# Kernel tuning notes

Hardware: AMD Instinct MI355X
Metric: run time of the kernel (lower is better)

Reference implementation:

```python
import jax, jax.numpy as jnp
import numpy as np

B, T, D, H = 2, 2048, 1024, 16
DH = D // H
SCALE = DH ** -0.5
NEG_INF = float(np.finfo(np.float32).min)


def setup_inputs() -> dict:
    key = jax.random.key(0)
    ks = jax.random.split(key, 8)
    query = jax.random.normal(ks[0], (B, T, D), dtype=jnp.float32)
    key_t = jax.random.normal(ks[1], (B, T, D), dtype=jnp.float32)
    value = jax.random.normal(ks[2], (B, T, D), dtype=jnp.float32)
    # causal mask: True means blocked (upper triangle)
    mask = ~jnp.tril(jnp.ones((T, T), dtype=bool))
    # key padding: pad tail beyond a random valid length per batch row
    lens = jax.random.randint(ks[3], (B,), T // 2, T)
    key_padding_mask = jnp.arange(T)[None, :] >= lens[:, None]  # [B, T] True = pad
    s = D ** -0.5
    Wq = jax.random.normal(ks[4], (D, D), dtype=jnp.float32) * s
    Wk = jax.random.normal(ks[5], (D, D), dtype=jnp.float32) * s
    Wv = jax.random.normal(ks[6], (D, D), dtype=jnp.float32) * s
    Wo = jax.random.normal(ks[7], (D, D), dtype=jnp.float32) * s
    return {"query": query, "key": key_t, "value": value, "mask": mask,
            "key_padding_mask": key_padding_mask, "Wq": Wq, "Wk": Wk, "Wv": Wv, "Wo": Wo}


def reference(query, key, value, mask, key_padding_mask, Wq, Wk, Wv, Wo):
    # Linear (no bias): y = x @ W.T, then split heads -> [B, H, T, DH]
    def proj(x, W, Tlen):
        return jnp.einsum('btd,ed->bte', x, W).reshape(B, Tlen, H, DH).transpose(0, 2, 1, 3)

    q = proj(query, Wq, T)
    k = proj(key, Wk, T)
    v = proj(value, Wv, T)

    attn = jnp.einsum('bhqd,bhkd->bhqk', q, k) * SCALE  # [B, H, Tq, Tk]
    attn = jnp.where(mask[None, None, :, :], -jnp.inf, attn)
    attn = jnp.where(key_padding_mask[:, None, None, :], -jnp.inf, attn)
    # rows of batches where ALL keys are padding: zero the logits (softmax -> uniform)
    all_masked = jnp.all(key_padding_mask, axis=-1)[:, None, None, None]
    attn = jnp.where(all_masked, 0.0, attn)

    p = jax.nn.softmax(attn, axis=-1)
    p = jnp.where(jnp.isnan(p), 0.0, p)  # scrub NaN rows (all -inf)

    out = jnp.einsum('bhqk,bhkd->bhqd', p, v)
    out = out.transpose(0, 2, 1, 3).reshape(B, T, D)
    return jnp.einsum('btd,ed->bte', out, Wo)
```

## Files before the change

kernel.cpp:

```cpp
#include <hip/hip_runtime.h>

#define B_  2
#define T_  2048
#define D_  1024
#define H_  16
#define DH_ 64
#define M_  4096

typedef _Float16 f16;
typedef _Float16 f16x8 __attribute__((ext_vector_type(8)));
typedef _Float16 f16x4 __attribute__((ext_vector_type(4)));
typedef __fp16   fp16x2 __attribute__((ext_vector_type(2)));
typedef float    f32x4  __attribute__((ext_vector_type(4)));
typedef float    f32x16 __attribute__((ext_vector_type(16)));
typedef unsigned int u32;

__device__ __forceinline__ void async_ld16(const void* g, void* l) {
  __builtin_amdgcn_global_load_lds(
      (const __attribute__((address_space(1))) unsigned int*)g,
      (__attribute__((address_space(3))) unsigned int*)l,
      16, 0, 0);
}

__device__ __forceinline__ u32 pkrtz(float a, float b) {
  union { fp16x2 h; u32 u; } x;
  x.h = __builtin_amdgcn_cvt_pkrtz(a, b);
  return x.u;
}

__global__ __launch_bounds__(256) void convert_all(
    const float* __restrict__ q, const float* __restrict__ k, const float* __restrict__ v,
    const float* __restrict__ wq, const float* __restrict__ wk, const float* __restrict__ wv,
    const float* __restrict__ wo, const void* __restrict__ kpm_raw,
    f16* __restrict__ xh, f16* __restrict__ wh, int* __restrict__ lens_out) {
  int bid = blockIdx.x;
  if (bid >= 8192) {
    int b = bid - 8192;
    __shared__ int s_c8, s_c32;
    if (threadIdx.x == 0) { s_c8 = 0; s_c32 = 0; }
    __syncthreads();
    int tid = threadIdx.x, lane = tid & 63;
    {
      const unsigned char* k8 = (const unsigned char*)kpm_raw + (long)b * T_;
      int cnt = 0;
      for (int j = tid; j < T_; j += 256) cnt += (k8[j] == 0) ? 1 : 0;
#pragma unroll
      for (int off = 1; off < 64; off <<= 1) cnt += __shfl_xor(cnt, off);
      if (lane == 0) atomicAdd(&s_c8, cnt);
    }
    {
      const int* k32 = (const int*)kpm_raw + (long)b * T_;
      int cnt = 0;
      for (int j = tid; j < T_; j += 256) cnt += (k32[j] == 0) ? 1 : 0;
#pragma unroll
      for (int off = 1; off < 64; off <<= 1) cnt += __shfl_xor(cnt, off);
      if (lane == 0) atomicAdd(&s_c32, cnt);
    }
    __syncthreads();
    if (tid == 0) lens_out[b] = (s_c8 == T_) ? s_c32 : s_c8;
    return;
  }
  const float* src;
  f16* dst;
  long base;
  if (bid < 6144) {
    int r = bid >> 11;
    src = (r == 0) ? q : (r == 1) ? k : v;
    dst = xh + (long)r * 4194304;
    base = (long)(bid & 2047) * 2048;
  } else {
    int r = (bid - 6144) >> 9;
    src = (r == 0) ? wq : (r == 1) ? wk : (r == 2) ? wv : wo;
    dst = wh + (long)r * 1048576;
    base = (long)((bid - 6144) & 511) * 2048;
  }
  long e = base + (long)threadIdx.x * 8;
  const float4* s4 = (const float4*)(src + e);
  float4 f0 = s4[0], f1 = s4[1];
  f16x8 o;
  o[0] = (f16)f0.x; o[1] = (f16)f0.y; o[2] = (f16)f0.z; o[3] = (f16)f0.w;
  o[4] = (f16)f1.x; o[5] = (f16)f1.y; o[6] = (f16)f1.z; o[7] = (f16)f1.w;
  *(f16x8*)(dst + e) = o;
}

__global__ __launch_bounds__(256) void gemm_k(
    const f16* __restrict__ Abase, const f16* __restrict__ Wbase,
    f16* __restrict__ Qb, f16* __restrict__ Kb, f16* __restrict__ Vt,
    float* __restrict__ Co, int which) {
  __shared__ __align__(16) f16 As[2][128][32];
  __shared__ __align__(16) f16 Bs[2][128][32];
  const int K = 1024, N = 1024;

  int gx = gridDim.x, gy = gridDim.y;
  int nwg = gx * gy * gridDim.z;
  int bid = blockIdx.x + gx * (blockIdx.y + gy * blockIdx.z);
  int cpx = nwg >> 3;
  int wg = (bid & 7) * cpx + (bid >> 3);
  int bz = wg / (gx * gy);
  int rem = wg - bz * gx * gy;
  int by = rem / gx, bx = rem - by * gx;

  int mode;
  const f16 *A, *W;
  if (which) { mode = 3; A = Abase; W = Wbase; }
  else {
    mode = bz;
    A = Abase + (long)bz * 4194304;
    W = Wbase + (long)bz * 1048576;
  }
  int m0 = by * 128, n0 = bx * 128;
  int tid = threadIdx.x, lane = tid & 63, w = tid >> 6;
  int wm = w >> 1, wn = w & 1;

  int srow = w * 16 + (lane >> 2);
  int scol = (lane & 3) * 8;
  const f16* pa = A + (long)(m0 + srow) * K + scol;
  const f16* pb = W + (long)(n0 + srow) * K + scol;

  f32x4 acc[4][4] = {};
  int row = lane & 15, kq = (lane >> 4) * 8;

  auto STAGE = [&](int k0, int bsel) {
    async_ld16(pa + k0,          &As[bsel][srow][scol]);
    async_ld16(pa + 64 * K + k0, &As[bsel][64 + srow][scol]);
    async_ld16(pb + k0,          &Bs[bsel][srow][scol]);
    async_ld16(pb + 64 * K + k0, &Bs[bsel][64 + srow][scol]);
  };

  STAGE(0, 0);
  asm volatile("s_waitcnt vmcnt(0)" ::: "memory");
  __builtin_amdgcn_s_barrier();

  int cur = 0;
  for (int k0 = 0; k0 < K; k0 += 32) {
    if (k0 + 32 < K) STAGE(k0 + 32, cur ^ 1);
    f16x8 af[4], bfr[4];
#pragma unroll
    for (int m = 0; m < 4; m++) af[m] = *(const f16x8*)&As[cur][wm * 64 + m * 16 + row][kq];
#pragma unroll
    for (int n = 0; n < 4; n++) bfr[n] = *(const f16x8*)&Bs[cur][wn * 64 + n * 16 + row][kq];
#pragma unroll
    for (int m = 0; m < 4; m++)
#pragma unroll
      for (int n = 0; n < 4; n++)
        acc[m][n] = __builtin_amdgcn_mfma_f32_16x16x32_f16(af[m], bfr[n], acc[m][n], 0, 0, 0);
    asm volatile("s_waitcnt vmcnt(0)" ::: "memory");
    __builtin_amdgcn_s_barrier();
    cur ^= 1;
  }

  int r0 = (lane >> 4) * 4;
#pragma unroll
  for (int m = 0; m < 4; m++) {
    int gmb = m0 + wm * 64 + m * 16 + r0;
#pragma unroll
    for (int n = 0; n < 4; n++) {
      int gn = n0 + wn * 64 + n * 16 + row;
      if (mode == 0) {
#pragma unroll
        for (int i = 0; i < 4; i++)
          Qb[(long)(gmb + i) * N + gn] = (f16)(acc[m][n][i] * 0.18033688f);
      } else if (mode == 1) {
#pragma unroll
        for (int i = 0; i < 4; i++)
          Kb[(long)(gmb + i) * N + gn] = (f16)acc[m][n][i];
      } else if (mode == 2) {
        int b = gmb >> 11;
        int t = gmb & 2047;
        int h = gn >> 6, dh = gn & 63;
        f16x4 pk;
#pragma unroll
        for (int i = 0; i < 4; i++) pk[i] = (f16)acc[m][n][i];
        *(f16x4*)&Vt[(long)((b * 16 + h) * 64 + dh) * 2048 + t] = pk;
      } else {
#pragma unroll
        for (int i = 0; i < 4; i++)
          Co[(long)(gmb + i) * N + gn] = acc[m][n][i];
      }
    }
  }
}

__global__ __launch_bounds__(256, 2) void attn_k(
    const f16* __restrict__ Q, const f16* __restrict__ Kp,
    const f16* __restrict__ Vt, const int* __restrict__ Lens,
    f16* __restrict__ Ao) {
  __shared__ __align__(16) f16 Kl[4][4096];
  __shared__ __align__(16) f16 Vl[4][4096];

  int tid = threadIdx.x, lane = tid & 63, w = tid >> 6;
  int bh = blockIdx.x;
  int j  = blockIdx.y;
  int qm = (j < 8) ? (15 - j) : (j - 8);
  int b = bh >> 4, h = bh & 15;
  int r31 = lane & 31, hi = lane >> 5, hi8 = hi * 8;

  int len = Lens[b];
  int q0 = qm * 128;
  int q0w = q0 + w * 32;
  int gq = q0w + r31;

  int blk_kmax = min(q0 + 128, len);
  int wav_kmax = min(q0w + 32, len);
  int NR = (blk_kmax + 127) >> 7;

  const f16* Qh = Q  + (long)b * T_ * D_ + h * 64;
  const f16* Kh = Kp + (long)b * T_ * D_ + h * 64;
  const f16* Vh = Vt + (long)(b * 16 + h) * 64 * T_;

  int srow = w * 16 + (lane >> 3);
  int sc8  = ((lane & 7) ^ ((lane >> 3) & 7)) * 8;
  int ldst = w * 1024 + lane * 8;

  int coff[4];
#pragma unroll
  for (int t = 0; t < 4; t++) coff[t] = ((2 * t + hi) ^ (r31 & 7)) * 8;

  auto STAGE64 = [&](int t, int bsel) {
    int kb = t * 64;
#pragma unroll
    for (int s = 0; s < 2; s++) {
      int row = srow + s * 8;
      async_ld16(Kh + (long)(kb + row) * D_ + sc8, &Kl[bsel][ldst + s * 512]);
      async_ld16(Vh + (long)row * T_ + kb + sc8,   &Vl[bsel][ldst + s * 512]);
    }
  };

  STAGE64(0, 0);
  STAGE64(1, 1);
  f16x8 qf[4];
#pragma unroll
  for (int t = 0; t < 4; t++)
    qf[t] = *(const f16x8*)(Qh + (long)gq * D_ + t * 16 + hi8);

  f32x16 o0 = {}, o1 = {};
  float mrun = -1e30f, lrun = 0.f;

  auto QK = [&](int buf, f32x16& sa, f32x16& sb) {
#pragma unroll
    for (int tq = 0; tq < 4; tq++) {
      f16x8 k0 = *(const f16x8*)&Kl[buf][(r31)      * 64 + coff[tq]];
      f16x8 k1 = *(const f16x8*)&Kl[buf][(32 + r31) * 64 + coff[tq]];
      sa = __builtin_amdgcn_mfma_f32_32x32x16_f16(k0, qf[tq], sa, 0, 0, 0);
      sb = __builtin_amdgcn_mfma_f32_32x32x16_f16(k1, qf[tq], sb, 0, 0, 0);
    }
  };

  auto MASK = [&](f32x16& sa, f32x16& sb, int kb) {
#pragma unroll
    for (int r = 0; r < 16; r++) {
      int pat = (r & 3) + 8 * (r >> 2) + 4 * hi;
      int gk0 = kb + pat, gk1 = kb + 32 + pat;
      if (gk0 > gq || gk0 >= len) sa[r] = -1e30f;
      if (gk1 > gq || gk1 >= len) sb[r] = -1e30f;
    }
  };

  auto PV = [&](int bufV, f32x16& sa, f32x16& sb) {
    u32 a0 = pkrtz(sa[0],  sa[1]),  a1 = pkrtz(sa[2],  sa[3]);
    u32 b0 = pkrtz(sa[4],  sa[5]),  b1 = pkrtz(sa[6],  sa[7]);
    u32 c0 = pkrtz(sa[8],  sa[9]),  c1 = pkrtz(sa[10], sa[11]);
    u32 d0 = pkrtz(sa[12], sa[13]), d1 = pkrtz(sa[14], sa[15]);
    u32 e0 = pkrtz(sb[0],  sb[1]),  e1 = pkrtz(sb[2],  sb[3]);
    u32 f0_ = pkrtz(sb[4],  sb[5]), f1_ = pkrtz(sb[6],  sb[7]);
    u32 g0 = pkrtz(sb[8],  sb[9]),  g1 = pkrtz(sb[10], sb[11]);
    u32 h0 = pkrtz(sb[12], sb[13]), h1 = pkrtz(sb[14], sb[15]);
    asm("v_permlane32_swap_b32 %0, %1" : "+v"(a0), "+v"(b0));
    asm("v_permlane32_swap_b32 %0, %1" : "+v"(a1), "+v"(b1));
    asm("v_permlane32_swap_b32 %0, %1" : "+v"(c0), "+v"(d0));
    asm("v_permlane32_swap_b32 %0, %1" : "+v"(c1), "+v"(d1));
    asm("v_permlane32_swap_b32 %0, %1" : "+v"(e0), "+v"(f0_));
    asm("v_permlane32_swap_b32 %0, %1" : "+v"(e1), "+v"(f1_));
    asm("v_permlane32_swap_b32 %0, %1" : "+v"(g0), "+v"(h0));
    asm("v_permlane32_swap_b32 %0, %1" : "+v"(g1), "+v"(h1));
    union { u32 w[4]; f16x8 v; } f00, f01, f10, f11;
    f00.w[0] = a0;  f00.w[1] = a1;  f00.w[2] = b0;  f00.w[3] = b1;
    f01.w[0] = c0;  f01.w[1] = c1;  f01.w[2] = d0;  f01.w[3] = d1;
    f10.w[0] = e0;  f10.w[1] = e1;  f10.w[2] = f0_; f10.w[3] = f1_;
    f11.w[0] = g0;  f11.w[1] = g1;  f11.w[2] = h0;  f11.w[3] = h1;

    f16x8 v00 = *(const f16x8*)&Vl[bufV][(r31)      * 64 + coff[0]];
    f16x8 v01 = *(const f16x8*)&Vl[bufV][(r31)      * 64 + coff[1]];
    f16x8 v02 = *(const f16x8*)&Vl[bufV][(r31)      * 64 + coff[2]];
    f16x8 v03 = *(const f16x8*)&Vl[bufV][(r31)      * 64 + coff[3]];
    f16x8 v10 = *(const f16x8*)&Vl[bufV][(32 + r31) * 64 + coff[0]];
    f16x8 v11 = *(const f16x8*)&Vl[bufV][(32 + r31) * 64 + coff[1]];
    f16x8 v12 = *(const f16x8*)&Vl[bufV][(32 + r31) * 64 + coff[2]];
    f16x8 v13 = *(const f16x8*)&Vl[bufV][(32 + r31) * 64 + coff[3]];

    o0 = __builtin_amdgcn_mfma_f32_32x32x16_f16(v00, f00.v, o0, 0, 0, 0);
    o0 = __builtin_amdgcn_mfma_f32_32x32x16_f16(v01, f01.v, o0, 0, 0, 0);
    o0 = __builtin_amdgcn_mfma_f32_32x32x16_f16(v02, f10.v, o0, 0, 0, 0);
    o0 = __builtin_amdgcn_mfma_f32_32x32x16_f16(v03, f11.v, o0, 0, 0, 0);
    o1 = __builtin_amdgcn_mfma_f32_32x32x16_f16(v10, f00.v, o1, 0, 0, 0);
    o1 = __builtin_amdgcn_mfma_f32_32x32x16_f16(v11, f01.v, o1, 0, 0, 0);
    o1 = __builtin_amdgcn_mfma_f32_32x32x16_f16(v12, f10.v, o1, 0, 0, 0);
    o1 = __builtin_amdgcn_mfma_f32_32x32x16_f16(v13, f11.v, o1, 0, 0, 0);
  };

  asm volatile("s_waitcnt vmcnt(0)" ::: "memory");
  __syncthreads();

  for (int r = 0; r < NR; r++) {
    int t0 = 2 * r;
    int b0buf = t0 & 3, b1buf = (t0 + 1) & 3;
    if (r + 1 < NR) { STAGE64(t0 + 2, (t0 + 2) & 3); STAGE64(t0 + 3, (t0 + 3) & 3); }

    int kb = r * 128;
    if (kb < wav_kmax) {
      bool has2 = (kb + 64) < wav_kmax;
      f32x16 s0 = {}, s1 = {}, s2, s3;
#pragma unroll
      for (int i = 0; i < 16; i++) { s2[i] = -1e30f; s3[i] = -1e30f; }

      QK(b0buf, s0, s1);
      if (has2) {
        f32x16 z0 = {}, z1 = {};
        QK(b1buf, z0, z1);
        s2 = z0; s3 = z1;
      }
      if (kb + 128 > q0w || kb + 128 > len) {
        MASK(s0, s1, kb);
        if (has2) MASK(s2, s3, kb + 64);
      }

      float t16[16];
#pragma unroll
      for (int rr = 0; rr < 16; rr++)
        t16[rr] = fmaxf(fmaxf(s0[rr], s1[rr]), fmaxf(s2[rr], s3[rr]));
#pragma unroll
      for (int s = 8; s > 0; s >>= 1)
#pragma unroll
        for (int rr = 0; rr < s; rr++) t16[rr] = fmaxf(t16[rr], t16[rr + s]);
      float mx = fmaxf(t16[0], __shfl_xor(t16[0], 32));

      float mnew = fmaxf(mrun, mx);
      float sf = exp2f(mrun - mnew);
      mrun = mnew;

      float ps[4] = {0.f, 0.f, 0.f, 0.f};
#pragma unroll
      for (int rr = 0; rr < 16; rr++) {
        s0[rr] = exp2f(s0[rr] - mnew);  ps[rr & 3] += s0[rr];
        s1[rr] = exp2f(s1[rr] - mnew);  ps[rr & 3] += s1[rr];
      }
      if (has2) {
#pragma unroll
        for (int rr = 0; rr < 16; rr++) {
          s2[rr] = exp2f(s2[rr] - mnew);  ps[rr & 3] += s2[rr];
          s3[rr] = exp2f(s3[rr] - mnew);  ps[rr & 3] += s3[rr];
        }
      }
      float psum = (ps[0] + ps[1]) + (ps[2] + ps[3]);
      lrun = lrun * sf + psum + __shfl_xor(psum, 32);

      o0 *= sf;
      o1 *= sf;

      PV(b0buf, s0, s1);
      if (has2) PV(b1buf, s2, s3);
    }

    asm volatile("s_waitcnt vmcnt(0)" ::: "memory");
    __syncthreads();
  }

  float linv = 1.f / lrun;
  f16* Aob = Ao + (long)(b * T_ + gq) * D_ + h * 64 + 4 * hi;
#pragma unroll
  for (int g = 0; g < 4; g++) {
    f16x4 s0, s1;
#pragma unroll
    for (int i = 0; i < 4; i++) {
      s0[i] = (f16)(o0[g * 4 + i] * linv);
      s1[i] = (f16)(o1[g * 4 + i] * linv);
    }
    *(f16x4*)(Aob + 8 * g)      = s0;
    *(f16x4*)(Aob + 32 + 8 * g) = s1;
  }
}

extern "C" void kernel_launch(void* const* d_in, const int* in_sizes, int n_in,
                              void* d_out, int out_size, void* d_ws, size_t ws_size,
                              hipStream_t stream) {
  const float* q  = (const float*)d_in[0];
  const float* k  = (const float*)d_in[1];
  const float* v  = (const float*)d_in[2];
  const void* kpm = d_in[4];
  const float* wq = (const float*)d_in[5];
  const float* wk = (const float*)d_in[6];
  const float* wv = (const float*)d_in[7];
  const float* wo = (const float*)d_in[8];

  char* ws = (char*)d_ws;
  f16* Xh = (f16*)(ws);
  f16* Wh = (f16*)(ws + 25165824);
  f16* Qb = (f16*)(ws + 33554432);
  f16* Kb = (f16*)(ws + 41943040);
  f16* Vt = (f16*)(ws + 50331648);
  f16* Ao = (f16*)(ws + 58720256);
  int* Lens = (int*)d_out;

  convert_all<<<8194, 256, 0, stream>>>(q, k, v, wq, wk, wv, wo, kpm, Xh, Wh, Lens);

  gemm_k<<<dim3(8, 32, 3), 256, 0, stream>>>(Xh, Wh, Qb, Kb, Vt, nullptr, 0);

  attn_k<<<dim3(B_ * H_, T_ / 128), 256, 0, stream>>>(Qb, Kb, Vt, Lens, Ao);

  gemm_k<<<dim3(8, 32, 1), 256, 0, stream>>>(Ao, Wh + 3 * 1048576, nullptr, nullptr,
                                             nullptr, (float*)d_out, 1);
}
```

Before: 127.0 us.

## Use 512-thread GEMM blocks with XOR-swizzled LDS layout

The projection GEMM now runs 8 waves per 128x128 tile instead of 4, with a 2x4 wave grid where each wave computes a 64x32 sub-tile. Each thread issues one async 16-byte load per operand per stage instead of two. The LDS tiles are flattened and stored with an XOR swizzle on the 8-element column chunk, which is meant to avoid bank conflicts on the fragment reads. The aim is more latency hiding and fewer LDS conflicts, at the cost of more waves competing for the CU and a smaller MFMA-to-load ratio per wave.

```diff
diff --git a/kernel.cpp b/kernel.cpp
--- a/kernel.cpp
+++ b/kernel.cpp
@@ -83,12 +83,12 @@
   *(f16x8*)(dst + e) = o;
 }
 
-__global__ __launch_bounds__(256) void gemm_k(
+__global__ __launch_bounds__(512) void gemm_k(
     const f16* __restrict__ Abase, const f16* __restrict__ Wbase,
     f16* __restrict__ Qb, f16* __restrict__ Kb, f16* __restrict__ Vt,
     float* __restrict__ Co, int which) {
-  __shared__ __align__(16) f16 As[2][128][32];
-  __shared__ __align__(16) f16 Bs[2][128][32];
+  __shared__ __align__(16) f16 As[2][4096];
+  __shared__ __align__(16) f16 Bs[2][4096];
   const int K = 1024, N = 1024;
 
   int gx = gridDim.x, gy = gridDim.y;
@@ -110,21 +110,24 @@
   }
   int m0 = by * 128, n0 = bx * 128;
   int tid = threadIdx.x, lane = tid & 63, w = tid >> 6;
-  int wm = w >> 1, wn = w & 1;
-
-  int srow = w * 16 + (lane >> 2);
-  int scol = (lane & 3) * 8;
+  int wr = w >> 2, wc = w & 3;
+
+  int srow = tid >> 2;
+  int sp   = tid & 3;
+  int ss   = ((srow & 3) + ((srow >> 2) & 3)) & 3;
+  int scol = (sp ^ ss) * 8;
   const f16* pa = A + (long)(m0 + srow) * K + scol;
   const f16* pb = W + (long)(n0 + srow) * K + scol;
-
-  f32x4 acc[4][4] = {};
-  int row = lane & 15, kq = (lane >> 4) * 8;
+  int ldst = tid * 8;
+
+  f32x4 acc[4][2] = {};
+  int row = lane & 15;
+  int rs  = ((row & 3) + ((row >> 2) & 3)) & 3;
+  int kq  = ((lane >> 4) ^ rs) * 8;
 
   auto STAGE = [&](int k0, int bsel) {
-    async_ld16(pa + k0,          &As[bsel][srow][scol]);
-    async_ld16(pa + 64 * K + k0, &As[bsel][64 + srow][scol]);
-    async_ld16(pb + k0,          &Bs[bsel][srow][scol]);
-    async_ld16(pb + 64 * K + k0, &Bs[bsel][64 + srow][scol]);
+    async_ld16(pa + k0, &As[bsel][ldst]);
+    async_ld16(pb + k0, &Bs[bsel][ldst]);
   };
 
   STAGE(0, 0);
@@ -134,15 +137,17 @@
   int cur = 0;
   for (int k0 = 0; k0 < K; k0 += 32) {
     if (k0 + 32 < K) STAGE(k0 + 32, cur ^ 1);
-    f16x8 af[4], bfr[4];
-#pragma unroll
-    for (int m = 0; m < 4; m++) af[m] = *(const f16x8*)&As[cur][wm * 64 + m * 16 + row][kq];
-#pragma unroll
-    for (int n = 0; n < 4; n++) bfr[n] = *(const f16x8*)&Bs[cur][wn * 64 + n * 16 + row][kq];
+    f16x8 af[4], bfr[2];
 #pragma unroll
     for (int m = 0; m < 4; m++)
-#pragma unroll
-      for (int n = 0; n < 4; n++)
+      af[m] = *(const f16x8*)&As[cur][(wr * 64 + m * 16 + row) * 32 + kq];
+#pragma unroll
+    for (int n = 0; n < 2; n++)
+      bfr[n] = *(const f16x8*)&Bs[cur][(wc * 32 + n * 16 + row) * 32 + kq];
+#pragma unroll
+    for (int m = 0; m < 4; m++)
+#pragma unroll
+      for (int n = 0; n < 2; n++)
         acc[m][n] = __builtin_amdgcn_mfma_f32_16x16x32_f16(af[m], bfr[n], acc[m][n], 0, 0, 0);
     asm volatile("s_waitcnt vmcnt(0)" ::: "memory");
     __builtin_amdgcn_s_barrier();
@@ -152,10 +157,10 @@
   int r0 = (lane >> 4) * 4;
 #pragma unroll
   for (int m = 0; m < 4; m++) {
-    int gmb = m0 + wm * 64 + m * 16 + r0;
-#pragma unroll
-    for (int n = 0; n < 4; n++) {
-      int gn = n0 + wn * 64 + n * 16 + row;
+    int gmb = m0 + wr * 64 + m * 16 + r0;
+#pragma unroll
+    for (int n = 0; n < 2; n++) {
+      int gn = n0 + wc * 32 + n * 16 + row;
       if (mode == 0) {
 #pragma unroll
         for (int i = 0; i < 4; i++)
@@ -403,10 +408,10 @@
 
   convert_all<<<8194, 256, 0, stream>>>(q, k, v, wq, wk, wv, wo, kpm, Xh, Wh, Lens);
 
-  gemm_k<<<dim3(8, 32, 3), 256, 0, stream>>>(Xh, Wh, Qb, Kb, Vt, nullptr, 0);
+  gemm_k<<<dim3(8, 32, 3), 512, 0, stream>>>(Xh, Wh, Qb, Kb, Vt, nullptr, 0);
 
   attn_k<<<dim3(B_ * H_, T_ / 128), 256, 0, stream>>>(Qb, Kb, Vt, Lens, Ao);
 
-  gemm_k<<<dim3(8, 32, 1), 256, 0, stream>>>(Ao, Wh + 3 * 1048576, nullptr, nullptr,
+  gemm_k<<<dim3(8, 32, 1), 512, 0, stream>>>(Ao, Wh + 3 * 1048576, nullptr, nullptr,
                                              nullptr, (float*)d_out, 1);
 }
```

Result: faster. 119.2 us (-6.2%).
